# Optimization experiments

Hardware: AMD Instinct MI355X
Metric: run time of the kernel (lower is better)

Reference implementation:

```python
import jax, jax.numpy as jnp
import numpy as np

D_Q = 512
D_O = 256  # = d_v = d_k = d_o
N_HEAD = 8
BN_EPS = 1e-5
LEAK = 0.1


def setup_inputs() -> dict:
    key = jax.random.key(0)
    ks = jax.random.split(key, 8)
    s = 0.02
    inp = {
        "q": jax.random.normal(ks[0], (64, D_Q), dtype=jnp.float32),
        "v": jax.random.normal(ks[1], (64, D_O, 32, 32), dtype=jnp.float32),
        "w_q": jax.random.normal(ks[2], (D_O, D_Q), dtype=jnp.float32) * s,
        "b_q": jnp.zeros((D_O,), jnp.float32),
        "w_kc": jax.random.normal(ks[3], (D_O, D_O), dtype=jnp.float32) * s,
        "b_kc": jnp.zeros((D_O,), jnp.float32),
        "w_kd": jax.random.normal(ks[4], (D_O, D_O), dtype=jnp.float32) * s,
        "b_kd": jnp.zeros((D_O,), jnp.float32),
        "w_v": jax.random.normal(ks[5], (D_O, D_O), dtype=jnp.float32) * s,
        "b_v": jnp.zeros((D_O,), jnp.float32),
        "temp_c": jnp.asarray(1.0, jnp.float32),
        "temp_d": jnp.asarray(1.0, jnp.float32),
        "bn_gamma": jnp.ones((D_O,), jnp.float32),
        "bn_beta": jnp.zeros((D_O,), jnp.float32),
        "bn_mean": jnp.zeros((D_O,), jnp.float32),
        "bn_var": jnp.ones((D_O,), jnp.float32),
    }
    return inp


def _conv1x1(x, wgt, bias):
    # x: (b, c, h, w), wgt: (o, c) -> (b, o, h, w)
    return jnp.einsum('bchw,oc->bohw', x, wgt) + bias[None, :, None, None]


def reference(q, v, w_q, b_q, w_kc, b_kc, w_kd, b_kd, w_v, b_v,
              temp_c, temp_d, bn_gamma, bn_beta, bn_mean, bn_var):
    b = q.shape[0]
    _, c_v, h, w = v.shape
    n = N_HEAD
    dh = D_O // n
    hw = h * w
    residual = v

    # projections
    qv = (q @ w_q.T + b_q).reshape(b, n, dh)                      # (b, n, dh)
    kc = _conv1x1(v, w_kc, b_kc).reshape(b, n, dh, hw).transpose(0, 1, 3, 2)  # (b, n, hw, dh)
    kd = _conv1x1(v, w_kd, b_kd).reshape(b, n, dh, hw).transpose(0, 1, 3, 2)
    vp = _conv1x1(v, w_v, b_v).reshape(b, n, dh, hw).transpose(0, 1, 3, 2)

    # collect: softmax attention with query length 1
    col_logit = jnp.einsum('bnd,bnsd->bns', qv, kc) / temp_c      # (b, n, hw)
    attn_col = jax.nn.softmax(col_logit, axis=2)
    attn = jnp.einsum('bns,bnsd->bnd', attn_col, vp)              # (b, n, dh)

    # diffuse: sigmoid gate, outer product with collected vector
    dif = jax.nn.sigmoid(jnp.einsum('bnsd,bnd->bns', kd, qv) / temp_d)  # (b, n, hw)
    out = jnp.einsum('bns,bnd->bnsd', dif, attn)                  # (b, n, hw, dh)

    # faithful to torch permute(0,1,4,3,2).view: swaps h and w (requires h==w)
    out = out.reshape(b, n, h, w, dh).transpose(0, 1, 4, 3, 2).reshape(b, D_O, w, h)
    out = out + residual

    # BatchNorm2d (eval: running stats) + LeakyReLU(0.1); dropout is identity at eval
    inv = bn_gamma / jnp.sqrt(bn_var + BN_EPS)
    out = (out - bn_mean[None, :, None, None]) * inv[None, :, None, None] + bn_beta[None, :, None, None]
    out = jnp.where(out >= 0, out, LEAK * out)
    return out
```

## Files before the change

### kernel.cpp

```cpp
#include <hip/hip_runtime.h>
#include <math.h>

#define B    64
#define DQ   512
#define DO   256
#define NH   8
#define DH   32
#define HW   1024
#define NCH  8
#define CHS  128

__global__ __launch_bounds__(256) void k1_qv(const float* __restrict__ q,
                                             const float* __restrict__ w_q,
                                             const float* __restrict__ b_q,
                                             float* __restrict__ qv) {
    int cg = blockIdx.x, b = blockIdx.y;
    int t = threadIdx.x;
    int wid = t >> 6, lane = t & 63;
    const float4* qrow = reinterpret_cast<const float4*>(q + (size_t)b*DQ);
    float4 q0 = qrow[lane*2], q1 = qrow[lane*2 + 1];
    #pragma unroll
    for (int r = 0; r < 4; ++r) {
        int c = cg*16 + wid*4 + r;
        const float4* wrow = reinterpret_cast<const float4*>(w_q + (size_t)c*DQ);
        float4 w0 = wrow[lane*2], w1 = wrow[lane*2 + 1];
        float acc = q0.x*w0.x + q0.y*w0.y + q0.z*w0.z + q0.w*w0.w
                  + q1.x*w1.x + q1.y*w1.y + q1.z*w1.z + q1.w*w1.w;
        #pragma unroll
        for (int k = 32; k > 0; k >>= 1) acc += __shfl_xor(acc, k);
        if (lane == 0) qv[b*DO + c] = acc + b_q[c];
    }
}

__global__ void k2_wqk(const float* __restrict__ qv,
                       const float* __restrict__ w_kc, const float* __restrict__ b_kc,
                       const float* __restrict__ w_kd, const float* __restrict__ b_kd,
                       const float* __restrict__ temp_c, const float* __restrict__ temp_d,
                       float* __restrict__ wqkc, float* __restrict__ wqkd,
                       float* __restrict__ qbc, float* __restrict__ qbd) {
    int bn = blockIdx.x;
    int n  = bn & 7;
    int t  = threadIdx.x;
    __shared__ float qvs[DH];
    if (t < DH) qvs[t] = qv[(bn >> 3)*DO + n*DH + t];
    __syncthreads();
    float itc = 1.0f / temp_c[0];
    float itd = 1.0f / temp_d[0];
    float ac = 0.f, ad = 0.f;
    #pragma unroll
    for (int d = 0; d < DH; ++d) {
        float qd = qvs[d];
        ac += qd * w_kc[(n*DH + d)*DO + t];
        ad += qd * w_kd[(n*DH + d)*DO + t];
    }
    wqkc[bn*DO + t] = ac * itc;
    wqkd[bn*DO + t] = ad * itd;
    if (t == 0) {
        float sc = 0.f;
        for (int d = 0; d < DH; ++d) sc += qvs[d]*b_kc[n*DH + d];
        qbc[bn] = sc * itc;
    }
    if (t == 1) {
        float sd = 0.f;
        for (int d = 0; d < DH; ++d) sd += qvs[d]*b_kd[n*DH + d];
        qbd[bn] = sd * itd;
    }
}

__global__ __launch_bounds__(512, 4)
void k3h(const float* __restrict__ v,
         const float* __restrict__ wqkc, const float* __restrict__ wqkd,
         const float* __restrict__ qbc,  const float* __restrict__ qbd,
         float* __restrict__ gate, float* __restrict__ pvp, float* __restrict__ mz) {
    __shared__ float pc[8*NH*CHS];
    __shared__ float pd[8*NH*CHS];
    __shared__ float e_lds[NH][CHS];
    int ch = blockIdx.x, b = blockIdx.y;
    int t  = threadIdx.x;
    int s0 = ch*CHS;
    int bn0 = b*NH;
    int lane = t & 63;
    int sl2  = lane*2;
    int csub = __builtin_amdgcn_readfirstlane(t >> 6);

    {
        const float* vb = v + (size_t)b*DO*HW + s0 + sl2;
        const float* wc = wqkc + (size_t)bn0*DO;
        const float* wd = wqkd + (size_t)bn0*DO;
        float acc_c0[NH] = {0,0,0,0,0,0,0,0}, acc_c1[NH] = {0,0,0,0,0,0,0,0};
        float acc_d0[NH] = {0,0,0,0,0,0,0,0}, acc_d1[NH] = {0,0,0,0,0,0,0,0};
        int cbase = csub*32;
        #pragma unroll 8
        for (int cc = 0; cc < 32; ++cc) {
            int c = cbase + cc;
            float2 v2 = *reinterpret_cast<const float2*>(vb + (size_t)c*HW);
            #pragma unroll
            for (int n = 0; n < NH; ++n) {
                float wcv = wc[n*DO + c];
                float wdv = wd[n*DO + c];
                acc_c0[n] = fmaf(wcv, v2.x, acc_c0[n]);
                acc_c1[n] = fmaf(wcv, v2.y, acc_c1[n]);
                acc_d0[n] = fmaf(wdv, v2.x, acc_d0[n]);
                acc_d1[n] = fmaf(wdv, v2.y, acc_d1[n]);
            }
        }
        #pragma unroll
        for (int n = 0; n < NH; ++n) {
            *reinterpret_cast<float2*>(&pc[(csub*NH + n)*CHS + sl2]) = make_float2(acc_c0[n], acc_c1[n]);
            *reinterpret_cast<float2*>(&pd[(csub*NH + n)*CHS + sl2]) = make_float2(acc_d0[n], acc_d1[n]);
        }
    }
    __syncthreads();

    {
        int n = csub;
        float lc0 = qbc[bn0+n], lc1 = lc0;
        float ld0 = qbd[bn0+n], ld1 = ld0;
        #pragma unroll
        for (int k = 0; k < 8; ++k) {
            float2 c2 = *reinterpret_cast<const float2*>(&pc[(k*NH + n)*CHS + sl2]);
            float2 d2 = *reinterpret_cast<const float2*>(&pd[(k*NH + n)*CHS + sl2]);
            lc0 += c2.x; lc1 += c2.y;
            ld0 += d2.x; ld1 += d2.y;
        }
        float g0 = 1.0f/(1.0f + __expf(-ld0));
        float g1 = 1.0f/(1.0f + __expf(-ld1));
        *reinterpret_cast<float2*>(gate + (size_t)(bn0+n)*HW + s0 + sl2) = make_float2(g0, g1);

        float m = fmaxf(lc0, lc1);
        #pragma unroll
        for (int k = 32; k > 0; k >>= 1) m = fmaxf(m, __shfl_xor(m, k));
        float e0 = __expf(lc0 - m), e1 = __expf(lc1 - m);
        float z = e0 + e1;
        #pragma unroll
        for (int k = 32; k > 0; k >>= 1) z += __shfl_xor(z, k);
        *reinterpret_cast<float2*>(&e_lds[n][sl2]) = make_float2(e0, e1);
        if (lane == 0) {
            float* mzp = mz + ((size_t)(b*NCH + ch)*NH + n)*2;
            mzp[0] = m; mzp[1] = z;
        }
    }
    __syncthreads();

    {
        int ng = t >> 8;
        int c  = t & 255;
        const float* vrow = v + ((size_t)(b*DO + c))*HW + s0;
        float a0 = 0.f, a1 = 0.f, a2 = 0.f, a3 = 0.f;
        #pragma unroll 4
        for (int j = 0; j < CHS/4; ++j) {
            float4 v4 = *reinterpret_cast<const float4*>(vrow + j*4);
            float4 e0 = *reinterpret_cast<const float4*>(&e_lds[ng*4+0][j*4]);
            float4 e1 = *reinterpret_cast<const float4*>(&e_lds[ng*4+1][j*4]);
            float4 e2 = *reinterpret_cast<const float4*>(&e_lds[ng*4+2][j*4]);
            float4 e3 = *reinterpret_cast<const float4*>(&e_lds[ng*4+3][j*4]);
            a0 += v4.x*e0.x + v4.y*e0.y + v4.z*e0.z + v4.w*e0.w;
            a1 += v4.x*e1.x + v4.y*e1.y + v4.z*e1.z + v4.w*e1.w;
            a2 += v4.x*e2.x + v4.y*e2.y + v4.z*e2.z + v4.w*e2.w;
            a3 += v4.x*e3.x + v4.y*e3.y + v4.z*e3.z + v4.w*e3.w;
        }
        size_t pb = ((size_t)(b*NCH + ch)*NH + ng*4)*DO + c;
        pvp[pb]        = a0;
        pvp[pb + DO]   = a1;
        pvp[pb + 2*DO] = a2;
        pvp[pb + 3*DO] = a3;
    }
}

__global__ void k4c(const float* __restrict__ pvp, const float* __restrict__ mz,
                    const float* __restrict__ w_v, const float* __restrict__ b_v,
                    float* __restrict__ attn) {
    __shared__ float scale[NCH][NH];
    __shared__ float pv_lds[NH*DO];
    int b = blockIdx.x, t = threadIdx.x;
    if (t < NH) {
        int n = t;
        float M = -1e30f;
        for (int ch = 0; ch < NCH; ++ch)
            M = fmaxf(M, mz[((size_t)(b*NCH+ch)*NH+n)*2]);
        float Z = 0.f;
        for (int ch = 0; ch < NCH; ++ch) {
            float sc = __expf(mz[((size_t)(b*NCH+ch)*NH+n)*2] - M);
            Z += sc * mz[((size_t)(b*NCH+ch)*NH+n)*2 + 1];
            scale[ch][n] = sc;
        }
        float inv = 1.0f/Z;
        for (int ch = 0; ch < NCH; ++ch) scale[ch][n] *= inv;
    }
    __syncthreads();
    #pragma unroll
    for (int r = 0; r < 2; ++r) {
        int i4 = t + r*256;
        int n  = i4 >> 6;
        float4 s = make_float4(0.f, 0.f, 0.f, 0.f);
        #pragma unroll
        for (int ch = 0; ch < NCH; ++ch) {
            float sc = scale[ch][n];
            float4 p = reinterpret_cast<const float4*>(pvp + (size_t)(b*NCH + ch)*NH*DO)[i4];
            s.x = fmaf(sc, p.x, s.x); s.y = fmaf(sc, p.y, s.y);
            s.z = fmaf(sc, p.z, s.z); s.w = fmaf(sc, p.w, s.w);
        }
        *reinterpret_cast<float4*>(&pv_lds[i4*4]) = s;
    }
    __syncthreads();
    int n = t >> 5;
    float acc = b_v[t];
    const float4* w4 = reinterpret_cast<const float4*>(w_v + t*DO);
    #pragma unroll 4
    for (int c4 = 0; c4 < DO/4; ++c4) {
        float4 wv = w4[c4];
        int c = c4*4;
        acc += pv_lds[n*DO+c]*wv.x + pv_lds[n*DO+c+1]*wv.y + pv_lds[n*DO+c+2]*wv.z + pv_lds[n*DO+c+3]*wv.w;
    }
    attn[b*DO + t] = acc;
}

__global__ void k5_out(const float* __restrict__ v, const float* __restrict__ gate,
                       const float* __restrict__ attn,
                       const float* __restrict__ bn_g, const float* __restrict__ bn_b,
                       const float* __restrict__ bn_m, const float* __restrict__ bn_v,
                       float* __restrict__ out) {
    int c = blockIdx.x, b = blockIdx.y;
    int n = c >> 5, d = c & 31;
    int t = threadIdx.x;
    __shared__ float g[32*33];
    float4 gv = reinterpret_cast<const float4*>(gate + (b*NH + n)*HW)[t];
    int s0 = t*4;
    int ga = s0 >> 5, gb = s0 & 31;
    g[ga*33 + gb + 0] = gv.x;
    g[ga*33 + gb + 1] = gv.y;
    g[ga*33 + gb + 2] = gv.z;
    g[ga*33 + gb + 3] = gv.w;
    __syncthreads();
    float av   = attn[(b*NH + n)*DH + d];
    float inv  = bn_g[c] / sqrtf(bn_v[c] + 1e-5f);
    float mean = bn_m[c], beta = bn_b[c];
    size_t base = ((size_t)(b*DO + c))*HW;
    float4 r4 = reinterpret_cast<const float4*>(v + base)[t];
    int l = 4*t;
    int i_ = l >> 5, j_ = l & 31;
    float x0 = g[(j_+0)*33 + i_]*av + r4.x;
    float x1 = g[(j_+1)*33 + i_]*av + r4.y;
    float x2 = g[(j_+2)*33 + i_]*av + r4.z;
    float x3 = g[(j_+3)*33 + i_]*av + r4.w;
    float y0 = (x0 - mean)*inv + beta; y0 = y0 >= 0.f ? y0 : 0.1f*y0;
    float y1 = (x1 - mean)*inv + beta; y1 = y1 >= 0.f ? y1 : 0.1f*y1;
    float y2 = (x2 - mean)*inv + beta; y2 = y2 >= 0.f ? y2 : 0.1f*y2;
    float y3 = (x3 - mean)*inv + beta; y3 = y3 >= 0.f ? y3 : 0.1f*y3;
    reinterpret_cast<float4*>(out + base)[t] = make_float4(y0, y1, y2, y3);
}

extern "C" void kernel_launch(void* const* d_in, const int* in_sizes, int n_in,
                              void* d_out, int out_size, void* d_ws, size_t ws_size,
                              hipStream_t stream) {
    const float* q      = (const float*)d_in[0];
    const float* v      = (const float*)d_in[1];
    const float* w_q    = (const float*)d_in[2];
    const float* b_q    = (const float*)d_in[3];
    const float* w_kc   = (const float*)d_in[4];
    const float* b_kc   = (const float*)d_in[5];
    const float* w_kd   = (const float*)d_in[6];
    const float* b_kd   = (const float*)d_in[7];
    const float* w_v    = (const float*)d_in[8];
    const float* b_v    = (const float*)d_in[9];
    const float* temp_c = (const float*)d_in[10];
    const float* temp_d = (const float*)d_in[11];
    const float* bn_g   = (const float*)d_in[12];
    const float* bn_b   = (const float*)d_in[13];
    const float* bn_m   = (const float*)d_in[14];
    const float* bn_v   = (const float*)d_in[15];
    float* out = (float*)d_out;

    float* ws   = (float*)d_ws;
    float* qv   = ws;
    float* wqkc = qv   + B*DO;
    float* wqkd = wqkc + B*NH*DO;
    float* qbc  = wqkd + B*NH*DO;
    float* qbd  = qbc  + B*NH;
    float* gate = qbd  + B*NH;
    float* mz   = gate + B*NH*HW;
    float* pvp  = mz   + B*NCH*NH*2;
    float* attn = pvp  + B*NCH*NH*DO;

    k1_qv <<<dim3(16, B),    256, 0, stream>>>(q, w_q, b_q, qv);
    k2_wqk<<<B*NH,           256, 0, stream>>>(qv, w_kc, b_kc, w_kd, b_kd, temp_c, temp_d,
                                               wqkc, wqkd, qbc, qbd);
    k3h   <<<dim3(NCH, B),   512, 0, stream>>>(v, wqkc, wqkd, qbc, qbd, gate, pvp, mz);
    k4c   <<<B,              256, 0, stream>>>(pvp, mz, w_v, b_v, attn);
    k5_out<<<dim3(DO, B),    256, 0, stream>>>(v, gate, attn, bn_g, bn_b, bn_m, bn_v, out);
}
```

Baseline: 77.41 us.

## Halve spatial chunk size and interleave projected key weights per channel

The spatial chunk shrinks from 128 to 64 positions, doubling the block count of the fused logit/softmax/partial-PV kernel to 1024 blocks. Each lane now handles one position instead of two. The query-projected key weights are stored interleaved as [b][c][16], so the collect and diffuse weights for a channel sit contiguously and can be fetched as wide uniform loads. The cost is twice as many partial PV vectors and (m,z) pairs for the combine kernel to reduce, plus less work per thread to hide latency.

```diff
diff --git a/kernel.cpp b/kernel.cpp
--- a/kernel.cpp
+++ b/kernel.cpp
@@ -7,8 +7,8 @@
 #define NH   8
 #define DH   32
 #define HW   1024
-#define NCH  8
-#define CHS  128
+#define NCH  16
+#define CHS  64
 
 __global__ __launch_bounds__(256) void k1_qv(const float* __restrict__ q,
                                              const float* __restrict__ w_q,
@@ -36,13 +36,14 @@
                        const float* __restrict__ w_kc, const float* __restrict__ b_kc,
                        const float* __restrict__ w_kd, const float* __restrict__ b_kd,
                        const float* __restrict__ temp_c, const float* __restrict__ temp_d,
-                       float* __restrict__ wqkc, float* __restrict__ wqkd,
-                       float* __restrict__ qbc, float* __restrict__ qbd) {
+                       float* __restrict__ wqkT, float* __restrict__ qbc,
+                       float* __restrict__ qbd) {
     int bn = blockIdx.x;
     int n  = bn & 7;
+    int bb = bn >> 3;
     int t  = threadIdx.x;
     __shared__ float qvs[DH];
-    if (t < DH) qvs[t] = qv[(bn >> 3)*DO + n*DH + t];
+    if (t < DH) qvs[t] = qv[bb*DO + n*DH + t];
     __syncthreads();
     float itc = 1.0f / temp_c[0];
     float itd = 1.0f / temp_d[0];
@@ -53,8 +54,8 @@
         ac += qd * w_kc[(n*DH + d)*DO + t];
         ad += qd * w_kd[(n*DH + d)*DO + t];
     }
-    wqkc[bn*DO + t] = ac * itc;
-    wqkd[bn*DO + t] = ad * itd;
+    wqkT[((size_t)bb*DO + t)*16 + n]     = ac * itc;
+    wqkT[((size_t)bb*DO + t)*16 + 8 + n] = ad * itd;
     if (t == 0) {
         float sc = 0.f;
         for (int d = 0; d < DH; ++d) sc += qvs[d]*b_kc[n*DH + d];
@@ -68,8 +69,8 @@
 }
 
 __global__ __launch_bounds__(512, 4)
-void k3h(const float* __restrict__ v,
-         const float* __restrict__ wqkc, const float* __restrict__ wqkd,
+void k3n(const float* __restrict__ v,
+         const float* __restrict__ wqkT,
          const float* __restrict__ qbc,  const float* __restrict__ qbd,
          float* __restrict__ gate, float* __restrict__ pvp, float* __restrict__ mz) {
     __shared__ float pc[8*NH*CHS];
@@ -80,61 +81,51 @@
     int s0 = ch*CHS;
     int bn0 = b*NH;
     int lane = t & 63;
-    int sl2  = lane*2;
     int csub = __builtin_amdgcn_readfirstlane(t >> 6);
 
     {
-        const float* vb = v + (size_t)b*DO*HW + s0 + sl2;
-        const float* wc = wqkc + (size_t)bn0*DO;
-        const float* wd = wqkd + (size_t)bn0*DO;
-        float acc_c0[NH] = {0,0,0,0,0,0,0,0}, acc_c1[NH] = {0,0,0,0,0,0,0,0};
-        float acc_d0[NH] = {0,0,0,0,0,0,0,0}, acc_d1[NH] = {0,0,0,0,0,0,0,0};
+        const float* vb = v + (size_t)b*DO*HW + s0 + lane;
+        const float* wt = wqkT + (size_t)b*DO*16;
+        float acc_c[NH] = {0,0,0,0,0,0,0,0};
+        float acc_d[NH] = {0,0,0,0,0,0,0,0};
         int cbase = csub*32;
         #pragma unroll 8
         for (int cc = 0; cc < 32; ++cc) {
             int c = cbase + cc;
-            float2 v2 = *reinterpret_cast<const float2*>(vb + (size_t)c*HW);
+            float vv = vb[(size_t)c*HW];
+            const float* wrow = wt + c*16;
             #pragma unroll
             for (int n = 0; n < NH; ++n) {
-                float wcv = wc[n*DO + c];
-                float wdv = wd[n*DO + c];
-                acc_c0[n] = fmaf(wcv, v2.x, acc_c0[n]);
-                acc_c1[n] = fmaf(wcv, v2.y, acc_c1[n]);
-                acc_d0[n] = fmaf(wdv, v2.x, acc_d0[n]);
-                acc_d1[n] = fmaf(wdv, v2.y, acc_d1[n]);
+                acc_c[n] = fmaf(wrow[n],     vv, acc_c[n]);
+                acc_d[n] = fmaf(wrow[8 + n], vv, acc_d[n]);
             }
         }
         #pragma unroll
         for (int n = 0; n < NH; ++n) {
-            *reinterpret_cast<float2*>(&pc[(csub*NH + n)*CHS + sl2]) = make_float2(acc_c0[n], acc_c1[n]);
-            *reinterpret_cast<float2*>(&pd[(csub*NH + n)*CHS + sl2]) = make_float2(acc_d0[n], acc_d1[n]);
+            pc[(csub*NH + n)*CHS + lane] = acc_c[n];
+            pd[(csub*NH + n)*CHS + lane] = acc_d[n];
         }
     }
     __syncthreads();
 
     {
         int n = csub;
-        float lc0 = qbc[bn0+n], lc1 = lc0;
-        float ld0 = qbd[bn0+n], ld1 = ld0;
+        float lc = qbc[bn0+n];
+        float ld = qbd[bn0+n];
         #pragma unroll
         for (int k = 0; k < 8; ++k) {
-            float2 c2 = *reinterpret_cast<const float2*>(&pc[(k*NH + n)*CHS + sl2]);
-            float2 d2 = *reinterpret_cast<const float2*>(&pd[(k*NH + n)*CHS + sl2]);
-            lc0 += c2.x; lc1 += c2.y;
-            ld0 += d2.x; ld1 += d2.y;
-        }
-        float g0 = 1.0f/(1.0f + __expf(-ld0));
-        float g1 = 1.0f/(1.0f + __expf(-ld1));
-        *reinterpret_cast<float2*>(gate + (size_t)(bn0+n)*HW + s0 + sl2) = make_float2(g0, g1);
-
-        float m = fmaxf(lc0, lc1);
+            lc += pc[(k*NH + n)*CHS + lane];
+            ld += pd[(k*NH + n)*CHS + lane];
+        }
+        gate[(size_t)(bn0+n)*HW + s0 + lane] = 1.0f/(1.0f + __expf(-ld));
+        float m = lc;
         #pragma unroll
         for (int k = 32; k > 0; k >>= 1) m = fmaxf(m, __shfl_xor(m, k));
-        float e0 = __expf(lc0 - m), e1 = __expf(lc1 - m);
-        float z = e0 + e1;
+        float e = __expf(lc - m);
+        e_lds[n][lane] = e;
+        float z = e;
         #pragma unroll
         for (int k = 32; k > 0; k >>= 1) z += __shfl_xor(z, k);
-        *reinterpret_cast<float2*>(&e_lds[n][sl2]) = make_float2(e0, e1);
         if (lane == 0) {
             float* mzp = mz + ((size_t)(b*NCH + ch)*NH + n)*2;
             mzp[0] = m; mzp[1] = z;
@@ -147,7 +138,7 @@
         int c  = t & 255;
         const float* vrow = v + ((size_t)(b*DO + c))*HW + s0;
         float a0 = 0.f, a1 = 0.f, a2 = 0.f, a3 = 0.f;
-        #pragma unroll 4
+        #pragma unroll
         for (int j = 0; j < CHS/4; ++j) {
             float4 v4 = *reinterpret_cast<const float4*>(vrow + j*4);
             float4 e0 = *reinterpret_cast<const float4*>(&e_lds[ng*4+0][j*4]);
@@ -193,7 +184,7 @@
         int i4 = t + r*256;
         int n  = i4 >> 6;
         float4 s = make_float4(0.f, 0.f, 0.f, 0.f);
-        #pragma unroll
+        #pragma unroll 4
         for (int ch = 0; ch < NCH; ++ch) {
             float sc = scale[ch][n];
             float4 p = reinterpret_cast<const float4*>(pvp + (size_t)(b*NCH + ch)*NH*DO)[i4];
@@ -273,19 +264,18 @@
 
     float* ws   = (float*)d_ws;
     float* qv   = ws;
-    float* wqkc = qv   + B*DO;
-    float* wqkd = wqkc + B*NH*DO;
-    float* qbc  = wqkd + B*NH*DO;
+    float* wqkT = qv   + B*DO;
+    float* qbc  = wqkT + (size_t)B*DO*16;
     float* qbd  = qbc  + B*NH;
     float* gate = qbd  + B*NH;
     float* mz   = gate + B*NH*HW;
     float* pvp  = mz   + B*NCH*NH*2;
-    float* attn = pvp  + B*NCH*NH*DO;
+    float* attn = pvp  + (size_t)B*NCH*NH*DO;
 
     k1_qv <<<dim3(16, B),    256, 0, stream>>>(q, w_q, b_q, qv);
     k2_wqk<<<B*NH,           256, 0, stream>>>(qv, w_kc, b_kc, w_kd, b_kd, temp_c, temp_d,
-                                               wqkc, wqkd, qbc, qbd);
-    k3h   <<<dim3(NCH, B),   512, 0, stream>>>(v, wqkc, wqkd, qbc, qbd, gate, pvp, mz);
+                                               wqkT, qbc, qbd);
+    k3n   <<<dim3(NCH, B),   512, 0, stream>>>(v, wqkT, qbc, qbd, gate, pvp, mz);
     k4c   <<<B,              256, 0, stream>>>(pvp, mz, w_v, b_v, attn);
     k5_out<<<dim3(DO, B),    256, 0, stream>>>(v, gate, attn, bn_g, bn_b, bn_m, bn_v, out);
 }
```

After: 83.83 us. 1.08x slower.
